# Optimization experiments

Measured on AMD Instinct MI355X. Metric: run time of the kernel, lower is better.

Reference implementation:

```python
import jax, jax.numpy as jnp
import numpy as np

INNER_DIM = 512
SCALE = 1.0 / np.sqrt(INNER_DIM).astype(np.float32)  # module scales by 1/sqrt(inner_dim), not head_dim


def setup_inputs() -> dict:
    key = jax.random.key(0)
    ks = jax.random.split(key, 7)
    b, n, d = 4, 4096, 512
    s = 0.02
    return {
        "x": jax.random.normal(ks[0], (b, n, d), jnp.float32),
        "y": jax.random.normal(ks[1], (b, n, d), jnp.float32),
        "Wq": jax.random.normal(ks[2], (INNER_DIM, d), jnp.float32) * s,  # torch Linear weight [out, in]
        "Wk": jax.random.normal(ks[3], (INNER_DIM, d), jnp.float32) * s,
        "Wv": jax.random.normal(ks[4], (INNER_DIM, d), jnp.float32) * s,
        "Wo": jax.random.normal(ks[5], (d, INNER_DIM), jnp.float32) * s,
        "bo": jax.random.normal(ks[6], (d,), jnp.float32) * s,
    }


def reference(x, y, Wq, Wk, Wv, Wo, bo):
    # q, k from x; v from y (bias-free projections)
    q = jnp.einsum('bnd,id->bni', x, Wq)
    k = jnp.einsum('bnd,id->bni', x, Wk)
    v = jnp.einsum('bnd,id->bni', y, Wv)
    # full [b, n, n] scores, scaled by 1/sqrt(inner_dim)
    alpha = jnp.einsum('bik,bjk->bij', q, k) * SCALE
    alpha = jax.nn.softmax(alpha, axis=-1)
    ctx = jnp.einsum('bij,bjd->bid', alpha, v)
    out = jnp.einsum('bid,od->bio', ctx, Wo) + bo
    return out
```

## Files before the change

### kernel.cpp

```cpp
#include <hip/hip_runtime.h>
#include <hip/hip_bf16.h>


typedef unsigned short u16;
typedef __bf16 bf16x8 __attribute__((ext_vector_type(8)));
typedef float f32x4 __attribute__((ext_vector_type(4)));

#define SCALE_QK 0.044194173824159216f

__device__ __forceinline__ u16 f2bf(float f) {
    __hip_bfloat16 h = __float2bfloat16(f);
    return __builtin_bit_cast(u16, h);
}

__device__ __forceinline__ void load_lds16(const void* g, void* l) {
    __builtin_amdgcn_global_load_lds(
        (const __attribute__((address_space(1))) void*)g,
        (__attribute__((address_space(3))) void*)l, 16, 0, 0);
}

__global__ void cvt_bf16_kernel(const float* __restrict__ src, u16* __restrict__ dst,
                                int n8, float scale) {
    int i = blockIdx.x * blockDim.x + threadIdx.x;
    if (i >= n8) return;
    const float4* s4 = (const float4*)src;
    float4 v0 = s4[2 * i], v1 = s4[2 * i + 1];
    union { u16 u[8]; uint4 v; } o;
    o.u[0] = f2bf(v0.x * scale); o.u[1] = f2bf(v0.y * scale);
    o.u[2] = f2bf(v0.z * scale); o.u[3] = f2bf(v0.w * scale);
    o.u[4] = f2bf(v1.x * scale); o.u[5] = f2bf(v1.y * scale);
    o.u[6] = f2bf(v1.z * scale); o.u[7] = f2bf(v1.w * scale);
    ((uint4*)dst)[i] = o.v;
}

__global__ void wvo_kernel(const float* __restrict__ Wo, const float* __restrict__ Wv,
                           float* __restrict__ Wvo) {
    int o = blockIdx.x, t = threadIdx.x;
    float a0 = 0.f, a1 = 0.f;
    for (int i = 0; i < 512; ++i) {
        float w = Wo[o * 512 + i];
        a0 += w * Wv[i * 512 + t];
        a1 += w * Wv[i * 512 + t + 256];
    }
    Wvo[o * 512 + t] = a0;
    Wvo[o * 512 + t + 256] = a1;
}

template <int EPI>
__launch_bounds__(256)
__global__ void gemm_bt_kernel(const u16* __restrict__ A, const u16* __restrict__ B,
                               void* __restrict__ Cout, int N, int K, int lda, int ldb,
                               long long sAz, long long sBz, long long sCz) {
    __shared__ u16 As[2][128 * 32];
    __shared__ u16 Bs[2][128 * 32];

    const int tid = threadIdx.x;
    const int wave = tid >> 6, lane = tid & 63;
    const int lr = lane & 15, lg = lane >> 4;
    const int wr = wave >> 1, wc = wave & 1;

    const int gx = gridDim.x, gy = gridDim.y;
    int bid = (blockIdx.z * gy + blockIdx.y) * gx + blockIdx.x;
    const int nwg = gx * gy * gridDim.z;
    int lgc = (bid & 7) * (nwg >> 3) + (bid >> 3);
    const int bx = lgc % gx;
    int rem = lgc / gx;
    const int by = rem % gy, z = rem / gy;
    const int row0 = by * 128, col0 = bx * 128;

    const u16* Ab = A + (size_t)z * sAz;
    const u16* Bb = B + (size_t)z * sBz;

    f32x4 acc[4][4];
#pragma unroll
    for (int i = 0; i < 4; ++i)
#pragma unroll
        for (int j = 0; j < 4; ++j) acc[i][j] = (f32x4){0.f, 0.f, 0.f, 0.f};

    const int KT = K >> 5;

#define STAGE(bufi, kt2)                                                          \
    {                                                                             \
        _Pragma("unroll") for (int i = 0; i < 2; ++i) {                           \
            int chunk = i * 256 + tid;                                            \
            int r = chunk >> 2, c4 = chunk & 3;                                   \
            load_lds16(Ab + (size_t)(row0 + r) * lda + (kt2) * 32 + c4 * 8,       \
                       &As[bufi][(i * 256 + wave * 64) * 8]);                     \
            load_lds16(Bb + (size_t)(col0 + r) * ldb + (kt2) * 32 + c4 * 8,       \
                       &Bs[bufi][(i * 256 + wave * 64) * 8]);                     \
        }                                                                         \
    }

    STAGE(0, 0);
    int buf = 0;
    for (int kt = 0; kt < KT; ++kt) {
        __syncthreads();
        if (kt + 1 < KT) STAGE(buf ^ 1, kt + 1);

        bf16x8 af[4], bfr[4];
#pragma unroll
        for (int mf = 0; mf < 4; ++mf)
            af[mf] = *(const bf16x8*)&As[buf][(wr * 64 + mf * 16 + lr) * 32 + lg * 8];
#pragma unroll
        for (int nf = 0; nf < 4; ++nf)
            bfr[nf] = *(const bf16x8*)&Bs[buf][(wc * 64 + nf * 16 + lr) * 32 + lg * 8];
#pragma unroll
        for (int mf = 0; mf < 4; ++mf)
#pragma unroll
            for (int nf = 0; nf < 4; ++nf)
                acc[mf][nf] = __builtin_amdgcn_mfma_f32_16x16x32_bf16(
                    af[mf], bfr[nf], acc[mf][nf], 0, 0, 0);
        buf ^= 1;
    }
#undef STAGE

    const int rbase = row0 + wr * 64;
    const int cbase = col0 + wc * 64;

    if (EPI == 0 || EPI == 2) {
        u16* C = (u16*)Cout + (size_t)z * sCz;
#pragma unroll
        for (int mf = 0; mf < 4; ++mf)
#pragma unroll
            for (int nf = 0; nf < 4; ++nf)
#pragma unroll
                for (int reg = 0; reg < 4; ++reg) {
                    int r = rbase + mf * 16 + lg * 4 + reg;
                    int c = cbase + nf * 16 + lr;
                    float v = acc[mf][nf][reg];
                    if (EPI == 2) v = __expf(v);
                    C[(size_t)r * N + c] = f2bf(v);
                }
    } else {
        u16* C = (u16*)Cout;
#pragma unroll
        for (int mf = 0; mf < 4; ++mf)
#pragma unroll
            for (int nf = 0; nf < 4; ++nf) {
                int rg = rbase + mf * 16 + lg * 4;
                int bsel = rg >> 12, rl = rg & 4095;
                int c = cbase + nf * 16 + lr;
                union { u16 u[4]; uint2 v; } o;
#pragma unroll
                for (int reg = 0; reg < 4; ++reg) o.u[reg] = f2bf(acc[mf][nf][reg]);
                *(uint2*)(C + ((size_t)bsel << 21) + ((size_t)c << 12) + rl) = o.v;
            }
    }
}

__launch_bounds__(512, 4)
__global__ void pv_kernel(const u16* __restrict__ P, const u16* __restrict__ vwT,
                          float* __restrict__ out, const float* __restrict__ bias) {
    __shared__ u16 As[2][64 * 32];
    __shared__ u16 Bs[2][512 * 32];
    __shared__ float lsh[64];

    const int tid = threadIdx.x;
    const int wave = tid >> 6, lane = tid & 63;
    const int lr = lane & 15, lg2 = lane >> 4;

    int bid = blockIdx.y * 64 + blockIdx.x;
    int lgc = (bid & 7) * 32 + (bid >> 3);
    const int rowpanel = lgc & 63, z = lgc >> 6;
    const int row0 = rowpanel * 64;

    const u16* Pz = P + (size_t)z * 16777216;
    const u16* Vz = vwT + (size_t)z * 2097152;
    float* Oz = out + (size_t)z * 2097152 + (size_t)row0 * 512;

    f32x4 acc[4][4];
#pragma unroll
    for (int i = 0; i < 4; ++i)
#pragma unroll
        for (int j = 0; j < 4; ++j) acc[i][j] = (f32x4){0.f, 0.f, 0.f, 0.f};
    float rs = 0.f;

#define STAGE(bufi, kt2)                                                          \
    {                                                                             \
        if (tid < 256) {                                                          \
            int r = tid >> 2, c4 = tid & 3;                                       \
            load_lds16(Pz + (size_t)(row0 + r) * 4096 + (kt2) * 32 + c4 * 8,      \
                       &As[bufi][wave * 512]);                                    \
        }                                                                         \
        _Pragma("unroll") for (int it = 0; it < 4; ++it) {                        \
            int c = it * 512 + tid;                                               \
            int r = c >> 2, c4 = c & 3;                                           \
            load_lds16(Vz + (size_t)r * 4096 + (kt2) * 32 + c4 * 8,               \
                       &Bs[bufi][(it * 512 + wave * 64) * 8]);                    \
        }                                                                         \
    }

    STAGE(0, 0);
    int buf = 0;
    for (int kt = 0; kt < 128; ++kt) {
        __syncthreads();
        if (kt + 1 < 128) STAGE(buf ^ 1, kt + 1);

        {
            uint2 rv = *(const uint2*)&As[buf][(tid >> 3) * 32 + (tid & 7) * 4];
            rs += __uint_as_float(rv.x << 16) + __uint_as_float(rv.x & 0xffff0000u) +
                  __uint_as_float(rv.y << 16) + __uint_as_float(rv.y & 0xffff0000u);
        }

        bf16x8 af[4];
#pragma unroll
        for (int mf = 0; mf < 4; ++mf)
            af[mf] = *(const bf16x8*)&As[buf][(mf * 16 + lr) * 32 + lg2 * 8];
#pragma unroll
        for (int nf = 0; nf < 4; ++nf) {
            bf16x8 bfr = *(const bf16x8*)&Bs[buf][(wave * 64 + nf * 16 + lr) * 32 + lg2 * 8];
#pragma unroll
            for (int mf = 0; mf < 4; ++mf)
                acc[mf][nf] = __builtin_amdgcn_mfma_f32_16x16x32_bf16(
                    af[mf], bfr, acc[mf][nf], 0, 0, 0);
        }
        buf ^= 1;
    }
#undef STAGE

    rs += __shfl_xor(rs, 1, 64);
    rs += __shfl_xor(rs, 2, 64);
    rs += __shfl_xor(rs, 4, 64);
    if ((tid & 7) == 0) lsh[tid >> 3] = rs;
    __syncthreads();

#pragma unroll
    for (int mf = 0; mf < 4; ++mf) {
        float4 lv = *(const float4*)&lsh[mf * 16 + lg2 * 4];
        float inv[4] = {1.f / lv.x, 1.f / lv.y, 1.f / lv.z, 1.f / lv.w};
#pragma unroll
        for (int nf = 0; nf < 4; ++nf) {
            int c = wave * 64 + nf * 16 + lr;
            float b = bias[c];
#pragma unroll
            for (int reg = 0; reg < 4; ++reg) {
                int r = mf * 16 + lg2 * 4 + reg;
                Oz[(size_t)r * 512 + c] = acc[mf][nf][reg] * inv[reg] + b;
            }
        }
    }
}

extern "C" void kernel_launch(void* const* d_in, const int* in_sizes, int n_in,
                              void* d_out, int out_size, void* d_ws, size_t ws_size,
                              hipStream_t stream) {
    const float* x  = (const float*)d_in[0];
    const float* y  = (const float*)d_in[1];
    const float* Wq = (const float*)d_in[2];
    const float* Wk = (const float*)d_in[3];
    const float* Wv = (const float*)d_in[4];
    const float* Wo = (const float*)d_in[5];
    const float* bo = (const float*)d_in[6];
    float* out = (float*)d_out;

    char* ws = (char*)d_ws;
    u16*   xb   = (u16*)(ws + 0);
    u16*   yb   = (u16*)(ws + 16777216);
    u16*   qk   = (u16*)(ws + 33554432);
    u16*   vwT  = (u16*)(ws + 67108864);
    u16*   Wqkb = (u16*)(ws + 83886080);
    u16*   Wvob = (u16*)(ws + 84934656);
    float* Wvo  = (float*)(ws + 85458944);
    u16*   P    = (u16*)(ws + 86507520);

    cvt_bf16_kernel<<<4096, 256, 0, stream>>>(x, xb, 1048576, 1.0f);
    cvt_bf16_kernel<<<4096, 256, 0, stream>>>(y, yb, 1048576, 1.0f);
    cvt_bf16_kernel<<<128, 256, 0, stream>>>(Wq, Wqkb, 32768, SCALE_QK);
    cvt_bf16_kernel<<<128, 256, 0, stream>>>(Wk, Wqkb + 262144, 32768, 1.0f);

    wvo_kernel<<<512, 256, 0, stream>>>(Wo, Wv, Wvo);
    cvt_bf16_kernel<<<128, 256, 0, stream>>>(Wvo, Wvob, 32768, 1.0f);

    gemm_bt_kernel<0><<<dim3(8, 128, 1), 256, 0, stream>>>(xb, Wqkb, qk,
                                                           1024, 512, 512, 512, 0, 0, 0);
    gemm_bt_kernel<1><<<dim3(4, 128, 1), 256, 0, stream>>>(yb, Wvob, vwT,
                                                           512, 512, 512, 512, 0, 0, 0);

    gemm_bt_kernel<2><<<dim3(32, 32, 4), 256, 0, stream>>>(qk, qk + 512, P,
                                                           4096, 512, 1024, 1024,
                                                           4194304, 4194304, 16777216);

    pv_kernel<<<dim3(64, 4, 1), 512, 0, stream>>>(P, vwT, out, bo);
}
```

Baseline: 345.6 us.

## Split PV kernel along K into two halves with a separate reduction kernel

The P·V kernel now splits the 4096-long reduction dimension into two halves, launching 512 blocks instead of 256. Each block writes unnormalized fp32 partial outputs and partial row sums to workspace. A new reduce kernel adds the halves, applies the softmax normalization and adds the bias. The goal is to fill more compute units, at the cost of extra global writes and reads of about 32MB of partials plus one more launch. The partial buffer reuses the xb/yb/qk workspace region, which is no longer needed by then.

```diff
diff --git a/kernel.cpp b/kernel.cpp
--- a/kernel.cpp
+++ b/kernel.cpp
@@ -150,23 +150,23 @@
 
 __launch_bounds__(512, 4)
 __global__ void pv_kernel(const u16* __restrict__ P, const u16* __restrict__ vwT,
-                          float* __restrict__ out, const float* __restrict__ bias) {
+                          float* __restrict__ part, float* __restrict__ lpart) {
     __shared__ u16 As[2][64 * 32];
     __shared__ u16 Bs[2][512 * 32];
-    __shared__ float lsh[64];
 
     const int tid = threadIdx.x;
     const int wave = tid >> 6, lane = tid & 63;
-    const int lr = lane & 15, lg2 = lane >> 4;
-
-    int bid = blockIdx.y * 64 + blockIdx.x;
-    int lgc = (bid & 7) * 32 + (bid >> 3);
-    const int rowpanel = lgc & 63, z = lgc >> 6;
-    const int row0 = rowpanel * 64;
-
-    const u16* Pz = P + (size_t)z * 16777216;
-    const u16* Vz = vwT + (size_t)z * 2097152;
-    float* Oz = out + (size_t)z * 2097152 + (size_t)row0 * 512;
+    const int lr = lane & 15, lg = lane >> 4;
+
+    int bid = blockIdx.x;
+    int lgc = (bid & 7) * 64 + (bid >> 3);
+    const int rp = lgc & 63;
+    const int ks = (lgc >> 6) & 1;
+    const int z = lgc >> 7;
+    const int row0 = rp * 64;
+
+    const u16* Pz = P + (size_t)z * 16777216 + (size_t)row0 * 4096 + ks * 2048;
+    const u16* Vz = vwT + (size_t)z * 2097152 + ks * 2048;
 
     f32x4 acc[4][4];
 #pragma unroll
@@ -179,7 +179,7 @@
     {                                                                             \
         if (tid < 256) {                                                          \
             int r = tid >> 2, c4 = tid & 3;                                       \
-            load_lds16(Pz + (size_t)(row0 + r) * 4096 + (kt2) * 32 + c4 * 8,      \
+            load_lds16(Pz + (size_t)r * 4096 + (kt2) * 32 + c4 * 8,               \
                        &As[bufi][wave * 512]);                                    \
         }                                                                         \
         _Pragma("unroll") for (int it = 0; it < 4; ++it) {                        \
@@ -192,9 +192,9 @@
 
     STAGE(0, 0);
     int buf = 0;
-    for (int kt = 0; kt < 128; ++kt) {
+    for (int kt = 0; kt < 64; ++kt) {
         __syncthreads();
-        if (kt + 1 < 128) STAGE(buf ^ 1, kt + 1);
+        if (kt + 1 < 64) STAGE(buf ^ 1, kt + 1);
 
         {
             uint2 rv = *(const uint2*)&As[buf][(tid >> 3) * 32 + (tid & 7) * 4];
@@ -205,10 +205,10 @@
         bf16x8 af[4];
 #pragma unroll
         for (int mf = 0; mf < 4; ++mf)
-            af[mf] = *(const bf16x8*)&As[buf][(mf * 16 + lr) * 32 + lg2 * 8];
+            af[mf] = *(const bf16x8*)&As[buf][(mf * 16 + lr) * 32 + lg * 8];
 #pragma unroll
         for (int nf = 0; nf < 4; ++nf) {
-            bf16x8 bfr = *(const bf16x8*)&Bs[buf][(wave * 64 + nf * 16 + lr) * 32 + lg2 * 8];
+            bf16x8 bfr = *(const bf16x8*)&Bs[buf][(wave * 64 + nf * 16 + lr) * 32 + lg * 8];
 #pragma unroll
             for (int mf = 0; mf < 4; ++mf)
                 acc[mf][nf] = __builtin_amdgcn_mfma_f32_16x16x32_bf16(
@@ -221,24 +221,39 @@
     rs += __shfl_xor(rs, 1, 64);
     rs += __shfl_xor(rs, 2, 64);
     rs += __shfl_xor(rs, 4, 64);
-    if ((tid & 7) == 0) lsh[tid >> 3] = rs;
-    __syncthreads();
-
-#pragma unroll
-    for (int mf = 0; mf < 4; ++mf) {
-        float4 lv = *(const float4*)&lsh[mf * 16 + lg2 * 4];
-        float inv[4] = {1.f / lv.x, 1.f / lv.y, 1.f / lv.z, 1.f / lv.w};
+    if ((tid & 7) == 0)
+        lpart[(size_t)ks * 16384 + z * 4096 + row0 + (tid >> 3)] = rs;
+
+    float* O = part + (size_t)ks * 8388608 + ((size_t)z * 4096 + row0) * 512;
+#pragma unroll
+    for (int mf = 0; mf < 4; ++mf)
 #pragma unroll
         for (int nf = 0; nf < 4; ++nf) {
             int c = wave * 64 + nf * 16 + lr;
-            float b = bias[c];
 #pragma unroll
             for (int reg = 0; reg < 4; ++reg) {
-                int r = mf * 16 + lg2 * 4 + reg;
-                Oz[(size_t)r * 512 + c] = acc[mf][nf][reg] * inv[reg] + b;
+                int r = mf * 16 + lg * 4 + reg;
+                O[(size_t)r * 512 + c] = acc[mf][nf][reg];
             }
         }
-    }
+}
+
+__global__ void reduce_kernel(const float* __restrict__ part,
+                              const float* __restrict__ lpart,
+                              const float* __restrict__ bo,
+                              float* __restrict__ out) {
+    int i = blockIdx.x * blockDim.x + threadIdx.x;
+    int r = i >> 7, c4 = i & 127;
+    float inv = 1.0f / (lpart[r] + lpart[16384 + r]);
+    float4 a = ((const float4*)part)[i];
+    float4 b = ((const float4*)part)[i + 2097152];
+    float4 bi = ((const float4*)bo)[c4];
+    float4 o;
+    o.x = (a.x + b.x) * inv + bi.x;
+    o.y = (a.y + b.y) * inv + bi.y;
+    o.z = (a.z + b.z) * inv + bi.z;
+    o.w = (a.w + b.w) * inv + bi.w;
+    ((float4*)out)[i] = o;
 }
 
 extern "C" void kernel_launch(void* const* d_in, const int* in_sizes, int n_in,
@@ -257,11 +272,13 @@
     u16*   xb   = (u16*)(ws + 0);
     u16*   yb   = (u16*)(ws + 16777216);
     u16*   qk   = (u16*)(ws + 33554432);
+    float* part = (float*)(ws + 0);
     u16*   vwT  = (u16*)(ws + 67108864);
     u16*   Wqkb = (u16*)(ws + 83886080);
     u16*   Wvob = (u16*)(ws + 84934656);
     float* Wvo  = (float*)(ws + 85458944);
-    u16*   P    = (u16*)(ws + 86507520);
+    float* lpart= (float*)(ws + 86507520);
+    u16*   P    = (u16*)(ws + 86638592);
 
     cvt_bf16_kernel<<<4096, 256, 0, stream>>>(x, xb, 1048576, 1.0f);
     cvt_bf16_kernel<<<4096, 256, 0, stream>>>(y, yb, 1048576, 1.0f);
@@ -280,5 +297,7 @@
                                                            4096, 512, 1024, 1024,
                                                            4194304, 4194304, 16777216);
 
-    pv_kernel<<<dim3(64, 4, 1), 512, 0, stream>>>(P, vwT, out, bo);
-}
+    pv_kernel<<<512, 512, 0, stream>>>(P, vwT, part, lpart);
+
+    reduce_kernel<<<8192, 256, 0, stream>>>(part, lpart, bo, out);
+}
```

New measurement: 318.1 us. 1.09x faster.
